# Kernel tuning notes

Hardware: AMD Instinct MI355X
Metric: run time of the kernel (lower is better)

Reference implementation:

```python
import jax, jax.numpy as jnp
import numpy as np

N, E, G = 100000, 400000, 4096
H, C = 4, 32            # heads, hidden_dim per head
D_OUT = H * C           # 128
NODE_D, EDGE_D = 38, 13
DEC_H, OUT_D = 64, 1
NEG_SLOPE = 0.2
LN_EPS = 1e-5


def setup_inputs() -> dict:
    key = jax.random.key(0)
    ks = jax.random.split(key, 40)
    r = lambda k, s: jax.random.normal(k, s, jnp.float32) * 0.1
    inp = {
        "x": jax.random.normal(ks[0], (N, NODE_D), jnp.float32),
        "edge_index": jax.random.randint(ks[1], (2, E), 0, N),
        "edge_attr": jax.random.uniform(ks[2], (E, EDGE_D), jnp.float32),
        "batch": jnp.sort(jax.random.randint(ks[3], (N,), 0, G)),
        # --- block 1 (in=38) ---
        "Wl1": r(ks[4], (NODE_D, D_OUT)), "bl1": jnp.zeros((D_OUT,), jnp.float32),
        "Wr1": r(ks[5], (NODE_D, D_OUT)), "br1": jnp.zeros((D_OUT,), jnp.float32),
        "We1": r(ks[6], (EDGE_D, D_OUT)),
        "att1": r(ks[7], (H, C)), "ab1": jnp.zeros((D_OUT,), jnp.float32),
        "ln_g1": jnp.ones((D_OUT,), jnp.float32), "ln_b1": jnp.zeros((D_OUT,), jnp.float32),
        "Wres": r(ks[8], (NODE_D, D_OUT)), "bres": jnp.zeros((D_OUT,), jnp.float32),
        # --- block 2 (in=128, residual = identity) ---
        "Wl2": r(ks[9], (D_OUT, D_OUT)), "bl2": jnp.zeros((D_OUT,), jnp.float32),
        "Wr2": r(ks[10], (D_OUT, D_OUT)), "br2": jnp.zeros((D_OUT,), jnp.float32),
        "We2": r(ks[11], (EDGE_D, D_OUT)),
        "att2": r(ks[12], (H, C)), "ab2": jnp.zeros((D_OUT,), jnp.float32),
        "ln_g2": jnp.ones((D_OUT,), jnp.float32), "ln_b2": jnp.zeros((D_OUT,), jnp.float32),
        # --- readout MLP ---
        "Wd1": r(ks[13], (D_OUT, DEC_H)), "bd1": jnp.zeros((DEC_H,), jnp.float32),
        "Wd2": r(ks[14], (DEC_H, OUT_D)), "bd2": jnp.zeros((OUT_D,), jnp.float32),
    }
    return inp


def _segment_softmax(logits, seg, n):
    m = jax.ops.segment_max(logits, seg, num_segments=n)
    ex = jnp.exp(logits - m[seg])
    s = jax.ops.segment_sum(ex, seg, num_segments=n)
    return ex / s[seg]


def _gatv2(x, src, dst, e_feat, Wl, bl, Wr, br, We, att, ab):
    n = x.shape[0]
    xl = (x @ Wl + bl).reshape(n, H, C)   # source transform
    xr = (x @ Wr + br).reshape(n, H, C)   # target transform
    ee = (e_feat @ We).reshape(-1, H, C)  # edge transform
    z = jax.nn.leaky_relu(xl[src] + xr[dst] + ee, NEG_SLOPE)  # [E,H,C]
    logits = jnp.einsum('ehc,hc->eh', z, att)                 # [E,H]
    alpha = _segment_softmax(logits, dst, n)                  # softmax over target nbhd
    out = jax.ops.segment_sum(xl[src] * alpha[..., None], dst, num_segments=n)
    return out.reshape(n, D_OUT) + ab


def _layernorm(h, g, b):
    mu = jnp.mean(h, -1, keepdims=True)
    d = h - mu
    v = jnp.mean(d * d, -1, keepdims=True)
    return d * jax.lax.rsqrt(v + LN_EPS) * g + b


def reference(x, edge_index, edge_attr, batch,
              Wl1, bl1, Wr1, br1, We1, att1, ab1, ln_g1, ln_b1, Wres, bres,
              Wl2, bl2, Wr2, br2, We2, att2, ab2, ln_g2, ln_b2,
              Wd1, bd1, Wd2, bd2):
    src, dst = edge_index[0], edge_index[1]
    n = x.shape[0]
    # add_self_loops(fill_value='mean'): self-loop edge attr = mean of incoming edge attrs
    deg = jax.ops.segment_sum(jnp.ones((src.shape[0],), x.dtype), dst, num_segments=n)
    loop_attr = jax.ops.segment_sum(edge_attr, dst, num_segments=n) / jnp.clip(deg, 1.0)[:, None]
    nodes = jnp.arange(n)
    src_a = jnp.concatenate([src, nodes])
    dst_a = jnp.concatenate([dst, nodes])
    ea = jnp.concatenate([edge_attr, loop_attr], axis=0)

    # block 1
    h = _gatv2(x, src_a, dst_a, ea, Wl1, bl1, Wr1, br1, We1, att1, ab1)
    h = jax.nn.elu(h)
    h = _layernorm(h + (x @ Wres + bres), ln_g1, ln_b1)
    # block 2 (identity residual)
    h2 = _gatv2(h, src_a, dst_a, ea, Wl2, bl2, Wr2, br2, We2, att2, ab2)
    h2 = jax.nn.elu(h2)
    h2 = _layernorm(h2 + h, ln_g2, ln_b2)

    # global mean pool over graphs
    cnt = jax.ops.segment_sum(jnp.ones((n,), x.dtype), batch, num_segments=G)
    g = jax.ops.segment_sum(h2, batch, num_segments=G) / jnp.clip(cnt, 1.0)[:, None]

    return jax.nn.relu(g @ Wd1 + bd1) @ Wd2 + bd2
```

## Files before the change

kernel.cpp:

```cpp
#include <hip/hip_runtime.h>

typedef unsigned short u16;
typedef unsigned int   u32;
typedef __attribute__((ext_vector_type(8))) short short8;
typedef __attribute__((ext_vector_type(4))) float float4v;
typedef __attribute__((ext_vector_type(2))) float float2v;

#define NODE_D   38
#define EDGE_D   13
#define D_OUT    128
#define NEG_SLOPE 0.2f
#define LN_EPS   1e-5f

__device__ __forceinline__ float bf2f(u16 v) { return __uint_as_float(((u32)v) << 16); }
__device__ __forceinline__ u16 f2bf(float f) {
    u32 u = __float_as_uint(f);
    u += 0x7fffu + ((u >> 16) & 1u);
    return (u16)(u >> 16);
}

__global__ void k_cnt(const int* __restrict__ dst, int E, int* __restrict__ deg,
                      const int* __restrict__ batch, int N, int* __restrict__ gcnt) {
    int i = blockIdx.x * blockDim.x + threadIdx.x;
    if (i < E) atomicAdd(deg + dst[i], 1);
    if (i < N) atomicAdd(gcnt + batch[i], 1);
}

#define SCAN_CHUNK 1024
__global__ void k_scan1(const int* __restrict__ cnt, int N, int addone, int* __restrict__ bsum) {
    __shared__ int sh[256];
    int base = blockIdx.x * SCAN_CHUNK;
    int t = threadIdx.x;
    int s = 0;
#pragma unroll
    for (int i = 0; i < 4; i++) { int idx = base + t * 4 + i; if (idx < N) s += cnt[idx] + addone; }
    sh[t] = s; __syncthreads();
    for (int ofs = 128; ofs > 0; ofs >>= 1) {
        if (t < ofs) sh[t] += sh[t + ofs];
        __syncthreads();
    }
    if (t == 0) bsum[blockIdx.x] = sh[0];
}
__global__ void k_scan2(const int* __restrict__ bsum, int nb, int* __restrict__ boff) {
    if (threadIdx.x == 0) {
        int run = 0;
        for (int i = 0; i < nb; i++) { boff[i] = run; run += bsum[i]; }
        boff[nb] = run;
    }
}
__global__ void k_scan3(const int* __restrict__ cnt, int N, int addone,
                        const int* __restrict__ boff, int nb, int* __restrict__ off) {
    __shared__ int wtot[4];
    int base = blockIdx.x * SCAN_CHUNK;
    int t = threadIdx.x;
    int lane = t & 63, w = t >> 6;
    int v[4]; int s = 0;
#pragma unroll
    for (int i = 0; i < 4; i++) { int idx = base + t * 4 + i; v[i] = (idx < N) ? cnt[idx] + addone : 0; s += v[i]; }
    int inc = s;
#pragma unroll
    for (int ofs = 1; ofs < 64; ofs <<= 1) {
        int x = __shfl_up(inc, ofs, 64);
        if (lane >= ofs) inc += x;
    }
    if (lane == 63) wtot[w] = inc;
    __syncthreads();
    int wofs = 0;
    for (int i = 0; i < w; i++) wofs += wtot[i];
    int run = boff[blockIdx.x] + wofs + (inc - s);
#pragma unroll
    for (int i = 0; i < 4; i++) {
        int idx = base + t * 4 + i;
        if (idx < N) off[idx] = run;
        run += v[i];
    }
    if (blockIdx.x == 0 && t == 0) off[N] = boff[nb];
}

__global__ void k_fill(const int* __restrict__ src, const int* __restrict__ dst,
                       const float* __restrict__ eattr, int E,
                       const int* __restrict__ csr_off, int* __restrict__ fill,
                       int* __restrict__ csr_src, u16* __restrict__ A) {
    int e = blockIdx.x * blockDim.x + threadIdx.x;
    if (e >= E) return;
    int d = dst[e];
    int pos = csr_off[d] + atomicAdd(fill + d, 1);
    csr_src[pos] = src[e];
    u16 row[16];
#pragma unroll
    for (int k = 0; k < EDGE_D; k++) row[k] = f2bf(eattr[(size_t)e * EDGE_D + k]);
#pragma unroll
    for (int k = EDGE_D; k < 16; k++) row[k] = 0;
    uint4* rp = (uint4*)(A + (size_t)pos * 16);
    rp[0] = (uint4){(u32)row[0] | ((u32)row[1] << 16), (u32)row[2] | ((u32)row[3] << 16),
                    (u32)row[4] | ((u32)row[5] << 16), (u32)row[6] | ((u32)row[7] << 16)};
    rp[1] = (uint4){(u32)row[8] | ((u32)row[9] << 16), (u32)row[10] | ((u32)row[11] << 16),
                    (u32)row[12] | ((u32)row[13] << 16), (u32)row[14] | ((u32)row[15] << 16)};
}

__global__ void k_self(const int* __restrict__ csr_off, int N,
                       int* __restrict__ csr_src, u16* __restrict__ A) {
    int tid = blockIdx.x * blockDim.x + threadIdx.x;
    if (tid >= N * 16) return;
    int n = tid >> 4, k = tid & 15;
    int b = csr_off[n], e2 = csr_off[n + 1] - 1;
    u16 v = 0;
    if (k < EDGE_D) {
        float s = 0.f;
        for (int j = b; j < e2; j++) s += bf2f(A[(size_t)j * 16 + k]);
        v = f2bf(s / fmaxf((float)(e2 - b), 1.f));
    }
    A[(size_t)e2 * 16 + k] = v;
    if (k == 0) csr_src[e2] = n;
}

template <int KPAD, int CT, int KREAL, bool IN_BF16>
__global__ __launch_bounds__(256) void k_tf_mfma(
    const void* __restrict__ in_v,
    const float* __restrict__ W0, const float* __restrict__ b0,
    const float* __restrict__ W1, const float* __restrict__ b1,
    const float* __restrict__ W2, const float* __restrict__ b2,
    u16* __restrict__ o0, u16* __restrict__ o1, u16* __restrict__ o2,
    int N) {
    constexpr int RS = KPAD + 8;
    __shared__ u16 Bsw[CT * 16 * RS];
    __shared__ float bsh[CT * 16];
    const float* Ws[3] = {W0, W1, W2};
    const float* bs[3] = {b0, b1, b2};
    u16* outs[3] = {o0, o1, o2};
    int t = threadIdx.x;
    for (int i = t; i < CT * 16 * KPAD; i += 256) {
        int c = i / KPAD, k = i - c * KPAD;
        float v = (k < KREAL) ? Ws[c >> 7][(size_t)k * 128 + (c & 127)] : 0.f;
        Bsw[c * RS + k] = f2bf(v);
    }
    for (int i = t; i < CT * 16; i += 256) bsh[i] = bs[i >> 7][i & 127];
    __syncthreads();

    int wid = t >> 6, lane = t & 63;
    int quad = lane >> 4, m = lane & 15;

    for (int g0 = blockIdx.x * 64; g0 < N; g0 += gridDim.x * 64) {
        int na = g0 + wid * 16 + m;
        if (na > N - 1) na = N - 1;
        short8 a[KPAD / 32];
        if (IN_BF16) {
            const u16* in = (const u16*)in_v;
#pragma unroll
            for (int kc = 0; kc < KPAD / 32; kc++)
                a[kc] = *(const short8*)(in + (size_t)na * KPAD + kc * 32 + quad * 8);
        } else {
            const float* in = (const float*)in_v;
#pragma unroll
            for (int kc = 0; kc < KPAD / 32; kc++)
#pragma unroll
                for (int j = 0; j < 8; j++) {
                    int k = kc * 32 + quad * 8 + j;
                    float v = (k < KREAL) ? in[(size_t)na * KREAL + k] : 0.f;
                    a[kc][j] = (short)f2bf(v);
                }
        }
        float4v acc[CT];
#pragma unroll
        for (int ct = 0; ct < CT; ct++) acc[ct] = (float4v){0.f, 0.f, 0.f, 0.f};
#pragma unroll
        for (int ct = 0; ct < CT; ct++) {
#pragma unroll
            for (int kc = 0; kc < KPAD / 32; kc++) {
                short8 b = *(const short8*)(&Bsw[(ct * 16 + m) * RS + kc * 32 + quad * 8]);
                acc[ct] = __builtin_amdgcn_mfma_f32_16x16x32_bf16(a[kc], b, acc[ct], 0, 0, 0);
            }
        }
#pragma unroll
        for (int ct = 0; ct < CT; ct++) {
            int col = ct * 16 + m;
            u16* op = outs[col >> 7];
            int cc = col & 127;
            float bv = bsh[col];
#pragma unroll
            for (int r = 0; r < 4; r++) {
                int node = g0 + wid * 16 + quad * 4 + r;
                if (node < N) op[(size_t)node * 128 + cc] = f2bf(acc[ct][r] + bv);
            }
        }
    }
}

__global__ __launch_bounds__(256) void k_gat(
    const int* __restrict__ csr_off, const int* __restrict__ csr_src,
    const u16* __restrict__ A_csr,
    const u16* __restrict__ xl, const u16* __restrict__ xr,
    const u16* __restrict__ res, const float* __restrict__ We,
    const float* __restrict__ att, const float* __restrict__ ab,
    const float* __restrict__ lng, const float* __restrict__ lnb,
    u16* __restrict__ hout, int N, int npw) {
    int t = threadIdx.x;
    int wid = t >> 6, lane = t & 63;
    int wave = blockIdx.x * 4 + wid;
    int n0 = wave * npw;
    if (n0 >= N) return;
    int n1 = n0 + npw; if (n1 > N) n1 = N;

    float2v we2[EDGE_D];
#pragma unroll
    for (int k = 0; k < EDGE_D; k++)
        we2[k] = (float2v){We[k * D_OUT + 2 * lane], We[k * D_OUT + 2 * lane + 1]};
    float a0 = att[2 * lane], a1 = att[2 * lane + 1];
    float abv0 = ab[2 * lane], abv1 = ab[2 * lane + 1];
    float lg0 = lng[2 * lane], lg1 = lng[2 * lane + 1];
    float lb0 = lnb[2 * lane], lb1 = lnb[2 * lane + 1];

    const u32* xl32 = (const u32*)xl;
    int wbeg = csr_off[n0];
    int wend = csr_off[n1];

    u32 xw = xl32[(size_t)csr_src[wbeg] * 64 + lane];
    const uint4* ap = (const uint4*)(A_csr + (size_t)wbeg * 16);
    uint4 aq0 = ap[0], aq1 = ap[1];

    int i = wbeg;
    for (int n = n0; n < n1; n++) {
        int end = csr_off[n + 1];
        u32 xrw = ((const u32*)xr)[(size_t)n * 64 + lane];
        float2v xr2 = (float2v){bf2f((u16)(xrw & 0xffff)), bf2f((u16)(xrw >> 16))};

        float ssum = 0.f;
        float2v acc2 = (float2v){0.f, 0.f};
        for (; i < end; i++) {
            u32 xwc = xw;
            uint4 q0 = aq0, q1 = aq1;
            if (i + 1 < wend) {
                xw = xl32[(size_t)csr_src[i + 1] * 64 + lane];
                const uint4* ap2 = (const uint4*)(A_csr + (size_t)(i + 1) * 16);
                aq0 = ap2[0]; aq1 = ap2[1];
            }
            u32 dw[8] = {q0.x, q0.y, q0.z, q0.w, q1.x, q1.y, q1.z, q1.w};
            float2v ee = (float2v){0.f, 0.f};
#pragma unroll
            for (int k = 0; k < EDGE_D; k++) {
                u32 d = dw[k >> 1];
                float av = bf2f((u16)((k & 1) ? (d >> 16) : (d & 0xffff)));
                ee += we2[k] * av;
            }
            float2v xs = (float2v){bf2f((u16)(xwc & 0xffff)), bf2f((u16)(xwc >> 16))};
            float2v z = xs + xr2 + ee;
            float z0 = z[0], z1 = z[1];
            z0 = (z0 > 0.f) ? z0 : z0 * NEG_SLOPE;
            z1 = (z1 > 0.f) ? z1 : z1 * NEG_SLOPE;
            float p = z0 * a0 + z1 * a1;
            p += __shfl_xor(p, 1, 64);
            p += __shfl_xor(p, 2, 64);
            p += __shfl_xor(p, 4, 64);
            p += __shfl_xor(p, 8, 64);
            float wgt = __expf(p);
            ssum += wgt;
            acc2 += xs * wgt;
        }

        float inv = 1.f / ssum;
        float o0 = acc2[0] * inv + abv0;
        float o1 = acc2[1] * inv + abv1;
        o0 = (o0 > 0.f) ? o0 : (__expf(o0) - 1.f);
        o1 = (o1 > 0.f) ? o1 : (__expf(o1) - 1.f);
        u32 rw = ((const u32*)res)[(size_t)n * 64 + lane];
        o0 += bf2f((u16)(rw & 0xffff));
        o1 += bf2f((u16)(rw >> 16));
        float sm = o0 + o1;
#pragma unroll
        for (int mk = 1; mk < 64; mk <<= 1) sm += __shfl_xor(sm, mk, 64);
        float mu = sm * (1.f / 128.f);
        float d0 = o0 - mu, d1 = o1 - mu;
        float vv = d0 * d0 + d1 * d1;
#pragma unroll
        for (int mk = 1; mk < 64; mk <<= 1) vv += __shfl_xor(vv, mk, 64);
        float rs = rsqrtf(vv * (1.f / 128.f) + LN_EPS);
        float h0 = d0 * rs * lg0 + lb0;
        float h1 = d1 * rs * lg1 + lb1;
        ((u32*)hout)[(size_t)n * 64 + lane] = (u32)f2bf(h0) | ((u32)f2bf(h1) << 16);
    }
}

__global__ __launch_bounds__(128) void k_pool_read(
    const u16* __restrict__ h2, const int* __restrict__ goff,
    const float* __restrict__ Wd1, const float* __restrict__ bd1,
    const float* __restrict__ Wd2, const float* __restrict__ bd2,
    float* __restrict__ out, int G) {
    __shared__ float psh[128];
    __shared__ float rsh[2][64];
    int g = blockIdx.x;
    int c = threadIdx.x;
    int b = goff[g], e = goff[g + 1];
    float s = 0.f;
    for (int n = b; n < e; n++) s += bf2f(h2[(size_t)n * 128 + c]);
    psh[c] = s / fmaxf((float)(e - b), 1.f);
    __syncthreads();
    int j = c & 63, hw = c >> 6;
    float acc = (hw == 0) ? bd1[j] : 0.f;
    int k0 = hw * 64;
    for (int k = k0; k < k0 + 64; k++)
        acc += psh[k] * Wd1[k * 64 + j];
    rsh[hw][j] = acc;
    __syncthreads();
    if (c < 64) {
        float a = fmaxf(rsh[0][c] + rsh[1][c], 0.f);
        float v = a * Wd2[c];
#pragma unroll
        for (int mk = 1; mk < 64; mk <<= 1) v += __shfl_xor(v, mk, 64);
        if (c == 0) out[g] = v + bd2[0];
    }
}

extern "C" void kernel_launch(void* const* d_in, const int* in_sizes, int n_in,
                              void* d_out, int out_size, void* d_ws, size_t ws_size,
                              hipStream_t stream) {
    const float* x     = (const float*)d_in[0];
    const int*   eidx  = (const int*)d_in[1];
    const float* eattr = (const float*)d_in[2];
    const int*   batch = (const int*)d_in[3];
    const float* Wl1 = (const float*)d_in[4],  *bl1 = (const float*)d_in[5];
    const float* Wr1 = (const float*)d_in[6],  *br1 = (const float*)d_in[7];
    const float* We1 = (const float*)d_in[8],  *att1 = (const float*)d_in[9],  *ab1 = (const float*)d_in[10];
    const float* lng1 = (const float*)d_in[11], *lnb1 = (const float*)d_in[12];
    const float* Wres = (const float*)d_in[13], *bres = (const float*)d_in[14];
    const float* Wl2 = (const float*)d_in[15], *bl2 = (const float*)d_in[16];
    const float* Wr2 = (const float*)d_in[17], *br2 = (const float*)d_in[18];
    const float* We2 = (const float*)d_in[19], *att2 = (const float*)d_in[20], *ab2 = (const float*)d_in[21];
    const float* lng2 = (const float*)d_in[22], *lnb2 = (const float*)d_in[23];
    const float* Wd1 = (const float*)d_in[24], *bd1 = (const float*)d_in[25];
    const float* Wd2 = (const float*)d_in[26], *bd2 = (const float*)d_in[27];

    int N = in_sizes[0] / NODE_D;
    int E = in_sizes[1] / 2;
    int G = out_size;
    int EN = E + N;
    const int* src = eidx;
    const int* dst = eidx + E;

    char* w = (char*)d_ws;
    auto alloc = [&](size_t bytes) -> char* {
        char* p = w;
        w += (bytes + 255) & ~(size_t)255;
        return p;
    };
    int NB  = (N + SCAN_CHUNK - 1) / SCAN_CHUNK;
    int NBG = (G + SCAN_CHUNK - 1) / SCAN_CHUNK;
    int*   csr_off  = (int*)alloc((size_t)(N + 1) * 4);
    int*   csr_src  = (int*)alloc((size_t)EN * 4);
    u16*   A_csr    = (u16*)alloc((size_t)(EN + 64) * 16 * 2);
    u16*   xlb      = (u16*)alloc((size_t)N * D_OUT * 2);
    u16*   xrb      = (u16*)alloc((size_t)N * D_OUT * 2);
    u16*   resb     = (u16*)alloc((size_t)N * D_OUT * 2);
    u16*   hb       = (u16*)alloc((size_t)N * D_OUT * 2);
    int*   gcnt     = (int*)alloc((size_t)G * 4);
    int*   gbsum    = (int*)alloc((size_t)NBG * 4);
    int*   gboff    = (int*)alloc((size_t)(NBG + 1) * 4);
    int*   goff     = (int*)alloc((size_t)(G + 1) * 4);
    int*   deg      = (int*)alloc((size_t)N * 4);
    int*   fill     = (int*)alloc((size_t)N * 4);
    int*   bsum     = (int*)alloc((size_t)(NB + 1) * 4);
    int*   boff     = (int*)alloc((size_t)(NB + 1) * 4);

    hipMemsetAsync(deg, 0, (size_t)N * 4, stream);
    hipMemsetAsync(fill, 0, (size_t)N * 4, stream);
    hipMemsetAsync(gcnt, 0, (size_t)G * 4, stream);

    k_cnt<<<(E + 255) / 256, 256, 0, stream>>>(dst, E, deg, batch, N, gcnt);

    k_scan1<<<NB, 256, 0, stream>>>(deg, N, 1, bsum);
    k_scan2<<<1, 64, 0, stream>>>(bsum, NB, boff);
    k_scan3<<<NB, 256, 0, stream>>>(deg, N, 1, boff, NB, csr_off);
    k_fill<<<(E + 255) / 256, 256, 0, stream>>>(src, dst, eattr, E, csr_off, fill, csr_src, A_csr);
    k_self<<<((size_t)N * 16 + 255) / 256, 256, 0, stream>>>(csr_off, N, csr_src, A_csr);

    k_scan1<<<NBG, 256, 0, stream>>>(gcnt, G, 0, gbsum);
    k_scan2<<<1, 64, 0, stream>>>(gbsum, NBG, gboff);
    k_scan3<<<NBG, 256, 0, stream>>>(gcnt, G, 0, gboff, NBG, goff);

    int npw = 4;
    int gblocks = (N + npw * 4 - 1) / (npw * 4);

    k_tf_mfma<64, 24, NODE_D, false><<<640, 256, 0, stream>>>(
        x, Wl1, bl1, Wr1, br1, Wres, bres, xlb, xrb, resb, N);
    k_gat<<<gblocks, 256, 0, stream>>>(csr_off, csr_src, A_csr,
                                       xlb, xrb, resb, We1, att1, ab1, lng1, lnb1, hb, N, npw);

    k_tf_mfma<128, 16, 128, true><<<640, 256, 0, stream>>>(
        hb, Wl2, bl2, Wr2, br2, Wr2, br2, xlb, xrb, xrb, N);
    k_gat<<<gblocks, 256, 0, stream>>>(csr_off, csr_src, A_csr,
                                       xlb, xrb, hb, We2, att2, ab2, lng2, lnb2, resb, N, npw);

    k_pool_read<<<G, 128, 0, stream>>>(resb, goff, Wd1, bd1, Wd2, bd2, (float*)d_out, G);
}
```

Before: 622.7 us.

## Double-buffer edge prefetch in GAT kernel and parallelize block-offset scan

The GAT aggregation loop now keeps two edges in flight (A/B register sets), prefetching the source row and edge attributes two edges ahead instead of one, and flattens the per-node loop into a single edge stream with node finalisation inline. This aims to hide more gather latency per wave. k_scan2 becomes a 256-thread shared-memory Hillis-Steele scan instead of a serial single-thread loop. The k_cnt grid is enlarged to cover max(E,N), presumably so every batch element gets counted. The change adds register pressure and more complex control flow.

```diff
diff --git a/kernel.cpp b/kernel.cpp
--- a/kernel.cpp
+++ b/kernel.cpp
@@ -42,7 +42,20 @@
     if (t == 0) bsum[blockIdx.x] = sh[0];
 }
 __global__ void k_scan2(const int* __restrict__ bsum, int nb, int* __restrict__ boff) {
-    if (threadIdx.x == 0) {
+    __shared__ int sh[256];
+    int t = threadIdx.x;
+    if (nb <= 256) {
+        int v = (t < nb) ? bsum[t] : 0;
+        sh[t] = v; __syncthreads();
+        for (int ofs = 1; ofs < 256; ofs <<= 1) {
+            int x = (t >= ofs) ? sh[t - ofs] : 0;
+            __syncthreads();
+            sh[t] += x;
+            __syncthreads();
+        }
+        if (t < nb) boff[t] = sh[t] - v;
+        if (t == nb - 1) boff[nb] = sh[t];
+    } else if (t == 0) {
         int run = 0;
         for (int i = 0; i < nb; i++) { boff[i] = run; run += bsum[i]; }
         boff[nb] = run;
@@ -213,50 +226,48 @@
     const u32* xl32 = (const u32*)xl;
     int wbeg = csr_off[n0];
     int wend = csr_off[n1];
-
-    u32 xw = xl32[(size_t)csr_src[wbeg] * 64 + lane];
-    const uint4* ap = (const uint4*)(A_csr + (size_t)wbeg * 16);
-    uint4 aq0 = ap[0], aq1 = ap[1];
-
+    int cl = wend - 1;
+
+    u32 xwA = xl32[(size_t)csr_src[wbeg] * 64 + lane];
+    const uint4* apA = (const uint4*)(A_csr + (size_t)wbeg * 16);
+    uint4 aA0 = apA[0], aA1 = apA[1];
+    int ib0 = (wbeg + 1 < wend) ? wbeg + 1 : cl;
+    u32 xwB = xl32[(size_t)csr_src[ib0] * 64 + lane];
+    const uint4* apB = (const uint4*)(A_csr + (size_t)ib0 * 16);
+    uint4 aB0 = apB[0], aB1 = apB[1];
+
+    int n = n0;
+    int end = csr_off[n + 1];
+    u32 xrw = ((const u32*)xr)[(size_t)n * 64 + lane];
+    float2v xr2 = (float2v){bf2f((u16)(xrw & 0xffff)), bf2f((u16)(xrw >> 16))};
+    float ssum = 0.f;
+    float2v acc2 = (float2v){0.f, 0.f};
     int i = wbeg;
-    for (int n = n0; n < n1; n++) {
-        int end = csr_off[n + 1];
-        u32 xrw = ((const u32*)xr)[(size_t)n * 64 + lane];
-        float2v xr2 = (float2v){bf2f((u16)(xrw & 0xffff)), bf2f((u16)(xrw >> 16))};
-
-        float ssum = 0.f;
-        float2v acc2 = (float2v){0.f, 0.f};
-        for (; i < end; i++) {
-            u32 xwc = xw;
-            uint4 q0 = aq0, q1 = aq1;
-            if (i + 1 < wend) {
-                xw = xl32[(size_t)csr_src[i + 1] * 64 + lane];
-                const uint4* ap2 = (const uint4*)(A_csr + (size_t)(i + 1) * 16);
-                aq0 = ap2[0]; aq1 = ap2[1];
-            }
-            u32 dw[8] = {q0.x, q0.y, q0.z, q0.w, q1.x, q1.y, q1.z, q1.w};
-            float2v ee = (float2v){0.f, 0.f};
-#pragma unroll
-            for (int k = 0; k < EDGE_D; k++) {
-                u32 d = dw[k >> 1];
-                float av = bf2f((u16)((k & 1) ? (d >> 16) : (d & 0xffff)));
-                ee += we2[k] * av;
-            }
-            float2v xs = (float2v){bf2f((u16)(xwc & 0xffff)), bf2f((u16)(xwc >> 16))};
-            float2v z = xs + xr2 + ee;
-            float z0 = z[0], z1 = z[1];
-            z0 = (z0 > 0.f) ? z0 : z0 * NEG_SLOPE;
-            z1 = (z1 > 0.f) ? z1 : z1 * NEG_SLOPE;
-            float p = z0 * a0 + z1 * a1;
-            p += __shfl_xor(p, 1, 64);
-            p += __shfl_xor(p, 2, 64);
-            p += __shfl_xor(p, 4, 64);
-            p += __shfl_xor(p, 8, 64);
-            float wgt = __expf(p);
-            ssum += wgt;
-            acc2 += xs * wgt;
-        }
-
+
+    auto edge = [&](u32 xwc, uint4 q0, uint4 q1) {
+        u32 dw[8] = {q0.x, q0.y, q0.z, q0.w, q1.x, q1.y, q1.z, q1.w};
+        float2v ee = (float2v){0.f, 0.f};
+#pragma unroll
+        for (int k = 0; k < EDGE_D; k++) {
+            u32 d = dw[k >> 1];
+            float av = bf2f((u16)((k & 1) ? (d >> 16) : (d & 0xffff)));
+            ee += we2[k] * av;
+        }
+        float2v xs = (float2v){bf2f((u16)(xwc & 0xffff)), bf2f((u16)(xwc >> 16))};
+        float2v z = xs + xr2 + ee;
+        float z0 = z[0], z1 = z[1];
+        z0 = (z0 > 0.f) ? z0 : z0 * NEG_SLOPE;
+        z1 = (z1 > 0.f) ? z1 : z1 * NEG_SLOPE;
+        float p = z0 * a0 + z1 * a1;
+        p += __shfl_xor(p, 1, 64);
+        p += __shfl_xor(p, 2, 64);
+        p += __shfl_xor(p, 4, 64);
+        p += __shfl_xor(p, 8, 64);
+        float wgt = __expf(p);
+        ssum += wgt;
+        acc2 += xs * wgt;
+    };
+    auto finalize = [&]() {
         float inv = 1.f / ssum;
         float o0 = acc2[0] * inv + abv0;
         float o1 = acc2[1] * inv + abv1;
@@ -277,6 +288,44 @@
         float h0 = d0 * rs * lg0 + lb0;
         float h1 = d1 * rs * lg1 + lb1;
         ((u32*)hout)[(size_t)n * 64 + lane] = (u32)f2bf(h0) | ((u32)f2bf(h1) << 16);
+    };
+    auto next_node = [&]() -> bool {
+        n++;
+        if (n >= n1) return false;
+        end = csr_off[n + 1];
+        u32 xw2 = ((const u32*)xr)[(size_t)n * 64 + lane];
+        xr2 = (float2v){bf2f((u16)(xw2 & 0xffff)), bf2f((u16)(xw2 >> 16))};
+        ssum = 0.f;
+        acc2 = (float2v){0.f, 0.f};
+        return true;
+    };
+
+    for (;;) {
+        edge(xwA, aA0, aA1);
+        {
+            int ip = (i + 2 < wend) ? i + 2 : cl;
+            xwA = xl32[(size_t)csr_src[ip] * 64 + lane];
+            const uint4* ap = (const uint4*)(A_csr + (size_t)ip * 16);
+            aA0 = ap[0]; aA1 = ap[1];
+        }
+        if (i + 1 == end) {
+            finalize();
+            if (!next_node()) break;
+        }
+        i++;
+        if (i >= wend) break;
+        edge(xwB, aB0, aB1);
+        {
+            int ip = (i + 2 < wend) ? i + 2 : cl;
+            xwB = xl32[(size_t)csr_src[ip] * 64 + lane];
+            const uint4* ap = (const uint4*)(A_csr + (size_t)ip * 16);
+            aB0 = ap[0]; aB1 = ap[1];
+        }
+        if (i + 1 == end) {
+            finalize();
+            if (!next_node()) break;
+        }
+        i++;
     }
 }
 
@@ -364,16 +413,17 @@
     hipMemsetAsync(fill, 0, (size_t)N * 4, stream);
     hipMemsetAsync(gcnt, 0, (size_t)G * 4, stream);
 
-    k_cnt<<<(E + 255) / 256, 256, 0, stream>>>(dst, E, deg, batch, N, gcnt);
+    int mx = (E > N) ? E : N;
+    k_cnt<<<(mx + 255) / 256, 256, 0, stream>>>(dst, E, deg, batch, N, gcnt);
 
     k_scan1<<<NB, 256, 0, stream>>>(deg, N, 1, bsum);
-    k_scan2<<<1, 64, 0, stream>>>(bsum, NB, boff);
+    k_scan2<<<1, 256, 0, stream>>>(bsum, NB, boff);
     k_scan3<<<NB, 256, 0, stream>>>(deg, N, 1, boff, NB, csr_off);
     k_fill<<<(E + 255) / 256, 256, 0, stream>>>(src, dst, eattr, E, csr_off, fill, csr_src, A_csr);
     k_self<<<((size_t)N * 16 + 255) / 256, 256, 0, stream>>>(csr_off, N, csr_src, A_csr);
 
     k_scan1<<<NBG, 256, 0, stream>>>(gcnt, G, 0, gbsum);
-    k_scan2<<<1, 64, 0, stream>>>(gbsum, NBG, gboff);
+    k_scan2<<<1, 256, 0, stream>>>(gbsum, NBG, gboff);
     k_scan3<<<NBG, 256, 0, stream>>>(gcnt, G, 0, gboff, NBG, goff);
 
     int npw = 4;
```

After: 645.1 us. 3.6% more time.
